# Optimization experiments

Measured on AMD Instinct MI355X. Metric: run time of the kernel, lower is better.

The kernel has to match this reference:

```python
import jax, jax.numpy as jnp
import numpy as np

B, S, D, H = 16, 1024, 768, 12
HD = D // H
SCALE = HD ** -0.5


def setup_inputs() -> dict:
    key = jax.random.key(0)
    k1, k2, k3, k4 = jax.random.split(key, 4)
    # Xavier-uniform-like init for the linear weights
    lim_qkv = (6.0 / (D + 3 * D)) ** 0.5
    lim_proj = (6.0 / (D + D)) ** 0.5
    return {
        "hidden_states": jax.random.normal(k1, (B, S, D), dtype=jnp.float32),
        "mask": jax.random.randint(k2, (B, S), 0, 2).astype(bool),
        "qkv_w": jax.random.uniform(k3, (3 * D, D), minval=-lim_qkv, maxval=lim_qkv, dtype=jnp.float32),
        "qkv_b": jnp.zeros((3 * D,), dtype=jnp.float32),
        "proj_w": jax.random.uniform(k4, (D, D), minval=-lim_proj, maxval=lim_proj, dtype=jnp.float32),
        "proj_b": jnp.zeros((D,), dtype=jnp.float32),
    }


def _masked_softmax(scores, attn_mask):
    # scores: [B,H,S,S]; attn_mask: [B,1,S,S] bool. Fully-masked rows -> all-zero
    # weights (torch gives NaN there but then zeroes the output rows; zeroing
    # the weights yields the identical final output without NaNs).
    neg_inf = jnp.finfo(scores.dtype).min
    m = jnp.max(jnp.where(attn_mask, scores, neg_inf), axis=-1, keepdims=True)
    e = jnp.where(attn_mask, jnp.exp(scores - m), 0.0)
    denom = jnp.sum(e, axis=-1, keepdims=True)
    return e / jnp.where(denom == 0, 1.0, denom)


def reference(hidden_states, mask, qkv_w, qkv_b, proj_w, proj_b):
    # fused QKV projection: [B,S,3D]
    qkv = hidden_states @ qkv_w.T + qkv_b
    qkv = qkv.reshape(B, S, 3, H, HD).transpose(2, 0, 3, 1, 4)  # [3,B,H,S,hd]
    q, k, v = qkv[0], qkv[1], qkv[2]
    tok_mask = mask[:, None, :, None]  # [B,1,S,1]
    q = jnp.where(tok_mask, q, 0.0)
    k = jnp.where(tok_mask, k, 0.0)
    v = jnp.where(tok_mask, v, 0.0)
    scores = jnp.einsum("bhqd,bhkd->bhqk", q, k) * SCALE
    attn_mask = (mask[:, :, None] & mask[:, None, :])[:, None]  # [B,1,S,S]
    attn = _masked_softmax(scores, attn_mask)
    context = jnp.einsum("bhqk,bhkd->bhqd", attn, v)
    context = context.transpose(0, 2, 1, 3).reshape(B, S, D)
    out = context @ proj_w.T + proj_b
    out = jnp.where(mask[:, :, None], out, 0.0)
    return out
```

## Files before the change

kernel.cpp:

```cpp
#include <hip/hip_runtime.h>
#include <cstdint>
#include <cstddef>

#define B 16
#define S 1024
#define D 768
#define H 12
#define HD 64
#define NTOK (B * S)
#define QKV_N (3 * D)
#define SCALE 0.125f
#define C2 2.88539008f
#define GK 768
#define NT_K 12

typedef _Float16 f16x8 __attribute__((ext_vector_type(8)));
typedef _Float16 f16x4 __attribute__((ext_vector_type(4)));
typedef __fp16 fp16x2 __attribute__((ext_vector_type(2)));
typedef float f32x4 __attribute__((ext_vector_type(4)));

typedef __attribute__((address_space(3))) void as3_void;
typedef const __attribute__((address_space(1))) void as1_void;

#if defined(__has_builtin)
#if __has_builtin(__builtin_amdgcn_exp2f)
#define EXP2(x) __builtin_amdgcn_exp2f(x)
#else
#define EXP2(x) exp2f(x)
#endif
#else
#define EXP2(x) exp2f(x)
#endif

__global__ __launch_bounds__(256) void normalize_mask_kernel(
    const unsigned char* __restrict__ raw, int* __restrict__ outm, int n) {
    __shared__ int s_isbyte;
    const int tid = threadIdx.x;
    if (tid == 0) s_isbyte = 0;
    __syncthreads();
    int found = 0;
    for (int i = tid; i < n; i += 256) {
        if ((i & 3) != 0 && raw[i] != 0) found = 1;
    }
    if (found) atomicOr(&s_isbyte, 1);
    __syncthreads();
    const int isbyte = s_isbyte;
    if (isbyte) {
        for (int i = tid; i < n; i += 256) outm[i] = raw[i] ? 1 : 0;
    } else {
        const int* r32 = (const int*)raw;
        for (int i = tid; i < n; i += 256) outm[i] = r32[i] ? 1 : 0;
    }
}

__global__ __launch_bounds__(256) void cvt_all_f16(
    const float* __restrict__ in0, _Float16* __restrict__ out0, int n0,
    const float* __restrict__ in1, _Float16* __restrict__ out1, int n1,
    const float* __restrict__ in2, _Float16* __restrict__ out2, int n2) {
    int i = blockIdx.x * 256 + threadIdx.x;
    const float* in;
    _Float16* out;
    if (i < n0) { in = in0; out = out0; }
    else if (i < n0 + n1) { i -= n0; in = in1; out = out1; }
    else { i -= n0 + n1; in = in2; out = out2; if (i >= n2) return; }
    const float4 v = ((const float4*)in)[i];
    f16x4 o;
    o[0] = (_Float16)v.x; o[1] = (_Float16)v.y;
    o[2] = (_Float16)v.z; o[3] = (_Float16)v.w;
    ((f16x4*)out)[i] = o;
}

template <int MODE>
__global__ __launch_bounds__(256, 2) void gemm16(
    const _Float16* __restrict__ A, const _Float16* __restrict__ Wm,
    const float* __restrict__ bias, const int* __restrict__ rowmask,
    int N, float* __restrict__ outf, _Float16* __restrict__ outh,
    _Float16* __restrict__ vtb) {
    __shared__ _Float16 smem[32768];

    const int tid = threadIdx.x;
    const int w = tid >> 6, l = tid & 63;
    const int wm = (w >> 1) * 64, wn = (w & 1) * 64;
    const int lg = l >> 4, lc = l & 15;

    const int bid = blockIdx.x;
    const int xcd = bid & 7;
    const int idx = bid >> 3;
    const int bn = (idx >> 4) * 128;
    const int bm = (xcd * 16 + (idx & 15)) * 128;

    f32x4 acc[4][4] = {};

#define STAGE(T, BUF)                                                           \
    {                                                                           \
        const int kt_ = (T) * 64;                                               \
        _Pragma("unroll")                                                       \
        for (int i_ = 0; i_ < 4; ++i_) {                                        \
            const int ci_ = (w << 2) + i_;                           \
            const int r_ = (ci_ << 3) + (l >> 3);                               \
            const int c16_ = (l & 7) ^ (r_ & 7);                                \
            __builtin_amdgcn_global_load_lds(                                   \
                (as1_void*)(A + (size_t)(bm + r_) * GK + kt_ + c16_ * 8),       \
                (as3_void*)(smem + (BUF) * 8192 + ci_ * 512), 16, 0, 0);        \
            __builtin_amdgcn_global_load_lds(                                   \
                (as1_void*)(Wm + (size_t)(bn + r_) * GK + kt_ + c16_ * 8),      \
                (as3_void*)(smem + 16384 + (BUF) * 8192 + ci_ * 512), 16, 0, 0);\
        }                                                                       \
    }

    STAGE(0, 0)

    for (int t = 0; t < NT_K; ++t) {
        const int cur = t & 1;
        if (t + 1 < NT_K) {
            STAGE(t + 1, cur ^ 1)
            asm volatile("s_waitcnt vmcnt(8)" ::: "memory");
        } else {
            asm volatile("s_waitcnt vmcnt(0)" ::: "memory");
        }
        __builtin_amdgcn_s_barrier();

        const _Float16* sA = smem + cur * 8192;
        const _Float16* sB = smem + 16384 + cur * 8192;
        __builtin_amdgcn_s_setprio(1);
#pragma unroll
        for (int kk = 0; kk < 2; ++kk) {
            const int c16 = ((kk << 2) + lg) ^ (lc & 7);
            f16x8 af[4], bf[4];
#pragma unroll
            for (int ni = 0; ni < 4; ++ni)
                bf[ni] = *(const f16x8*)&sB[(wn + ni * 16 + lc) * 64 + c16 * 8];
#pragma unroll
            for (int mi = 0; mi < 4; ++mi)
                af[mi] = *(const f16x8*)&sA[(wm + mi * 16 + lc) * 64 + c16 * 8];
#pragma unroll
            for (int mi = 0; mi < 4; ++mi)
#pragma unroll
                for (int ni = 0; ni < 4; ++ni)
                    acc[mi][ni] = __builtin_amdgcn_mfma_f32_16x16x32_f16(
                        af[mi], bf[ni], acc[mi][ni], 0, 0, 0);
        }
        __builtin_amdgcn_s_setprio(0);
        __builtin_amdgcn_s_barrier();
    }
#undef STAGE

    float bs[4];
#pragma unroll
    for (int ni = 0; ni < 4; ++ni) bs[ni] = bias[bn + wn + ni * 16 + lc];

    if (MODE == 1) {
        if (bn < 1536) {
#pragma unroll
            for (int mi = 0; mi < 4; ++mi) {
#pragma unroll
                for (int j = 0; j < 4; ++j) {
                    const int m = bm + wm + mi * 16 + lg * 4 + j;
#pragma unroll
                    for (int ni = 0; ni < 4; ++ni) {
                        const int col = bn + wn + ni * 16 + lc;
                        outh[(size_t)m * N + col] =
                            (_Float16)(acc[mi][ni][j] + bs[ni]);
                    }
                }
            }
        } else {
#pragma unroll
            for (int mi = 0; mi < 4; ++mi) {
#pragma unroll
                for (int ni = 0; ni < 4; ++ni) {
                    f16x4 v4;
#pragma unroll
                    for (int j = 0; j < 4; ++j)
                        v4[j] = (_Float16)(acc[mi][ni][j] + bs[ni]);
                    const int nl = wn + ni * 16 + lc;
                    const int ml = wm + mi * 16 + lg * 4;
                    *(f16x4*)&smem[nl * 136 + ml] = v4;
                }
            }
            __syncthreads();
            const int r = tid >> 1;
            const int c0 = (tid & 1) * 64;
            const int col0 = bn - 1536 + r;
            const int hh = col0 >> 6, hd = col0 & 63;
            const int bb = bm >> 10;
            const int s0 = (bm & 1023) + c0;
            _Float16* dst = vtb + ((size_t)(bb * H + hh) * HD + hd) * S + s0;
#pragma unroll
            for (int e = 0; e < 8; ++e)
                *(f16x8*)(dst + e * 8) = *(const f16x8*)&smem[r * 136 + c0 + e * 8];
        }
    } else {
#pragma unroll
        for (int mi = 0; mi < 4; ++mi) {
#pragma unroll
            for (int j = 0; j < 4; ++j) {
                const int m = bm + wm + mi * 16 + lg * 4 + j;
                const int mv = rowmask[m];
#pragma unroll
                for (int ni = 0; ni < 4; ++ni) {
                    const int col = bn + wn + ni * 16 + lc;
                    outf[(size_t)m * N + col] = mv ? acc[mi][ni][j] + bs[ni] : 0.f;
                }
            }
        }
    }
}

__global__ __launch_bounds__(256, 3) void attn_kernel(
    const _Float16* __restrict__ qkv, const _Float16* __restrict__ vtb,
    const int* __restrict__ mask, _Float16* __restrict__ ctx) {
    __shared__ _Float16 ksm[2][64 * 64];
    __shared__ _Float16 vsm[2][64 * 64];
    __shared__ float mbias[S];

    const int blk = blockIdx.x;
    const int xcd = blk & 7;
    const int idx = blk >> 3;
    const int bh_ = xcd * 24 + (idx >> 2);
    const int qt = idx & 3;
    const int h = bh_ % H;
    const int b = bh_ / H;
    const int tid = threadIdx.x;
    const int w = tid >> 6, lane = tid & 63;
    const int lg = lane >> 4, lc = lane & 15;

    const size_t bh = (size_t)(b * H + h);
    const _Float16* Kp = qkv + (size_t)(b * S) * QKV_N + D + h * HD;
    const _Float16* Vt = vtb + bh * HD * S;
    const int* mrow = mask + b * S;

    const int r0 = w * 8 + (lane >> 3);
    const int swz8 = ((lane & 7) ^ (r0 & 7)) * 8;
    const int koff0 = r0 * QKV_N + swz8;
    const int koff1 = (32 + r0) * QKV_N + swz8;
    const int voff0 = r0 * S + swz8;
    const int voff1 = (32 + r0) * S + swz8;

#define STAGE(KT, BUF)                                                         \
    {                                                                          \
        __builtin_amdgcn_global_load_lds(                                      \
            (as1_void*)(Kp + (size_t)(KT) * QKV_N + koff0),                    \
            (as3_void*)(&ksm[BUF][w * 512]), 16, 0, 0);                        \
        __builtin_amdgcn_global_load_lds(                                      \
            (as1_void*)(Kp + (size_t)(KT) * QKV_N + koff1),                    \
            (as3_void*)(&ksm[BUF][2048 + w * 512]), 16, 0, 0);                 \
        __builtin_amdgcn_global_load_lds(                                      \
            (as1_void*)(Vt + (size_t)(KT) + voff0),                            \
            (as3_void*)(&vsm[BUF][w * 512]), 16, 0, 0);                        \
        __builtin_amdgcn_global_load_lds(                                      \
            (as1_void*)(Vt + (size_t)(KT) + voff1),                            \
            (as3_void*)(&vsm[BUF][2048 + w * 512]), 16, 0, 0);                 \
    }

    const int qbase = qt * 256 + w * 16 + lc;
    const _Float16 qs = (_Float16)(0.125f * 1.44269504f);
    f16x8 qf[4][2];
#pragma unroll
    for (int qg = 0; qg < 4; ++qg) {
        const _Float16* Qp =
            qkv + (size_t)(b * S + qbase + qg * 64) * QKV_N + h * HD;
        qf[qg][0] = *(const f16x8*)(Qp + lg * 8);
        qf[qg][1] = *(const f16x8*)(Qp + 32 + lg * 8);
        qf[qg][0] *= qs;
        qf[qg][1] *= qs;
    }

#pragma unroll
    for (int i = 0; i < 4; ++i)
        mbias[i * 256 + tid] = mrow[i * 256 + tid] ? -C2 : -1e9f;

    STAGE(0, 0)
    __syncthreads();

    f32x4 acc[4][4] = {};
    float lsum[4] = {0.f, 0.f, 0.f, 0.f};
    fp16x2 ones;
    ones[0] = (__fp16)1.0f; ones[1] = (__fp16)1.0f;

    for (int it = 0; it < S / 64; ++it) {
        const int cur = it & 1;
        if (it + 1 < S / 64) STAGE((it + 1) * 64, cur ^ 1)

        __builtin_amdgcn_s_setprio(1);
#pragma unroll
        for (int t = 0; t < 4; ++t) {
            const int krow = (t * 16 + lc) * 64;
            const f16x8 kfa =
                *(const f16x8*)&ksm[cur][krow + (lg ^ (lc & 7)) * 8];
            const f16x8 kfb =
                *(const f16x8*)&ksm[cur][krow + ((4 + lg) ^ (lc & 7)) * 8];
            const f32x4 mb = *(const f32x4*)&mbias[it * 64 + t * 16 + 4 * lg];

            f16x4 pp[4];
#pragma unroll
            for (int qg = 0; qg < 4; ++qg) {
                f32x4 c = mb;
                c = __builtin_amdgcn_mfma_f32_16x16x32_f16(kfa, qf[qg][0], c, 0, 0, 0);
                c = __builtin_amdgcn_mfma_f32_16x16x32_f16(kfb, qf[qg][1], c, 0, 0, 0);
                const auto u0 = __builtin_amdgcn_cvt_pkrtz(EXP2(c[0]), EXP2(c[1]));
                const auto u1 = __builtin_amdgcn_cvt_pkrtz(EXP2(c[2]), EXP2(c[3]));
                lsum[qg] = __builtin_amdgcn_fdot2(u0, ones, lsum[qg], false);
                lsum[qg] = __builtin_amdgcn_fdot2(u1, ones, lsum[qg], false);
                pp[qg][0] = (_Float16)u0[0]; pp[qg][1] = (_Float16)u0[1];
                pp[qg][2] = (_Float16)u1[0]; pp[qg][3] = (_Float16)u1[1];
            }

#pragma unroll
            for (int g = 0; g < 4; ++g) {
                const int vrow = (g * 16 + lc) * 64;
                const f16x4 vf = *(const f16x4*)&vsm[cur][
                    vrow + (((2 * t + (lg >> 1)) ^ (lc & 7)) << 3) + (lg & 1) * 4];
#pragma unroll
                for (int qg = 0; qg < 4; ++qg)
                    acc[qg][g] = __builtin_amdgcn_mfma_f32_16x16x16f16(
                        pp[qg], vf, acc[qg][g], 0, 0, 0);
            }
        }
        __builtin_amdgcn_s_setprio(0);
        __syncthreads();
    }
#undef STAGE

#pragma unroll
    for (int qg = 0; qg < 4; ++qg) {
        float l = lsum[qg];
        l += __shfl_xor(l, 16);
        l += __shfl_xor(l, 32);
        const float inv = l > 0.f ? 1.f / l : 0.f;
#pragma unroll
        for (int j = 0; j < 4; ++j) {
            const int qin = 4 * lg + j;
            const float ij = __shfl(inv, qin);
            const int qr = qt * 256 + qg * 64 + w * 16 + qin;
            const float iq = mrow[qr] ? ij : 0.f;
            const size_t o = ((size_t)(b * S + qr)) * D + h * HD;
#pragma unroll
            for (int g = 0; g < 4; ++g)
                ctx[o + 16 * g + lc] = (_Float16)(acc[qg][g][j] * iq);
        }
    }
}

extern "C" void kernel_launch(void* const* d_in, const int* in_sizes, int n_in,
                              void* d_out, int out_size, void* d_ws, size_t ws_size,
                              hipStream_t stream) {
    const float* hidden = (const float*)d_in[0];
    const unsigned char* maskraw = (const unsigned char*)d_in[1];
    const float* qkv_w = (const float*)d_in[2];
    const float* qkv_b = (const float*)d_in[3];
    const float* proj_w = (const float*)d_in[4];
    const float* proj_b = (const float*)d_in[5];
    float* out = (float*)d_out;

    char* ws = (char*)d_ws;
    size_t off = 0;
    int* maskN = (int*)(ws + off);            off += (size_t)NTOK * 4;
    _Float16* hid16 = (_Float16*)(ws + off);  off += (size_t)NTOK * D * 2;
    _Float16* qkvw16 = (_Float16*)(ws + off); off += (size_t)QKV_N * D * 2;
    _Float16* projw16 = (_Float16*)(ws + off); off += (size_t)D * D * 2;
    _Float16* qkv16 = (_Float16*)(ws + off);  off += (size_t)NTOK * QKV_N * 2;
    _Float16* vt = (_Float16*)(ws + off);     off += (size_t)NTOK * D * 2;
    _Float16* ctx16 = (_Float16*)(ws + off);  off += (size_t)NTOK * D * 2;

    normalize_mask_kernel<<<1, 256, 0, stream>>>(maskraw, maskN, NTOK);

    const int n0 = NTOK * D / 4, n1 = QKV_N * D / 4, n2 = D * D / 4;
    cvt_all_f16<<<(n0 + n1 + n2 + 255) / 256, 256, 0, stream>>>(
        hidden, hid16, n0, qkv_w, qkvw16, n1, proj_w, projw16, n2);

    gemm16<1><<<dim3(2304), 256, 0, stream>>>(
        hid16, qkvw16, qkv_b, nullptr, QKV_N, nullptr, qkv16, vt);

    attn_kernel<<<dim3(B * H * (S / 256)), 256, 0, stream>>>(qkv16, vt, maskN, ctx16);

    gemm16<0><<<dim3(768), 256, 0, stream>>>(
        ctx16, projw16, proj_b, maskN, D, out, nullptr, nullptr);
}
```

Measured before the change: 206.7 us.

## Triple-buffer K/V tiles in attention with explicit vmcnt waits

Moves the attention kernel's K/V shared-memory staging from double to triple buffering. It prefetches two tiles ahead and replaces __syncthreads with explicit s_waitcnt vmcnt levels plus raw s_barrier, so more global-load latency overlaps the MFMA work. The GEMM barriers also switch to inline-asm s_barrier. The cost is an extra 16KB of LDS per block, which may reduce occupancy under launch_bounds(256,3), and hand-tuned waitcnt counts that must match the number of loads in flight.

```diff
diff --git a/kernel.cpp b/kernel.cpp
--- a/kernel.cpp
+++ b/kernel.cpp
@@ -31,6 +31,8 @@
 #else
 #define EXP2(x) exp2f(x)
 #endif
+
+#define BARRIER() asm volatile("s_barrier" ::: "memory")
 
 __global__ __launch_bounds__(256) void normalize_mask_kernel(
     const unsigned char* __restrict__ raw, int* __restrict__ outm, int n) {
@@ -118,7 +120,7 @@
         } else {
             asm volatile("s_waitcnt vmcnt(0)" ::: "memory");
         }
-        __builtin_amdgcn_s_barrier();
+        BARRIER();
 
         const _Float16* sA = smem + cur * 8192;
         const _Float16* sB = smem + 16384 + cur * 8192;
@@ -141,7 +143,7 @@
                         af[mi], bf[ni], acc[mi][ni], 0, 0, 0);
         }
         __builtin_amdgcn_s_setprio(0);
-        __builtin_amdgcn_s_barrier();
+        BARRIER();
     }
 #undef STAGE
 
@@ -210,8 +212,8 @@
 __global__ __launch_bounds__(256, 3) void attn_kernel(
     const _Float16* __restrict__ qkv, const _Float16* __restrict__ vtb,
     const int* __restrict__ mask, _Float16* __restrict__ ctx) {
-    __shared__ _Float16 ksm[2][64 * 64];
-    __shared__ _Float16 vsm[2][64 * 64];
+    __shared__ _Float16 ksm[3][64 * 64];
+    __shared__ _Float16 vsm[3][64 * 64];
     __shared__ float mbias[S];
 
     const int blk = blockIdx.x;
@@ -237,19 +239,20 @@
     const int voff0 = r0 * S + swz8;
     const int voff1 = (32 + r0) * S + swz8;
 
-#define STAGE(KT, BUF)                                                         \
+#define STAGE(T, BUF)                                                          \
     {                                                                          \
+        const int kt_ = (T) * 64;                                              \
         __builtin_amdgcn_global_load_lds(                                      \
-            (as1_void*)(Kp + (size_t)(KT) * QKV_N + koff0),                    \
+            (as1_void*)(Kp + (size_t)kt_ * QKV_N + koff0),                     \
             (as3_void*)(&ksm[BUF][w * 512]), 16, 0, 0);                        \
         __builtin_amdgcn_global_load_lds(                                      \
-            (as1_void*)(Kp + (size_t)(KT) * QKV_N + koff1),                    \
+            (as1_void*)(Kp + (size_t)kt_ * QKV_N + koff1),                     \
             (as3_void*)(&ksm[BUF][2048 + w * 512]), 16, 0, 0);                 \
         __builtin_amdgcn_global_load_lds(                                      \
-            (as1_void*)(Vt + (size_t)(KT) + voff0),                            \
+            (as1_void*)(Vt + (size_t)kt_ + voff0),                            \
             (as3_void*)(&vsm[BUF][w * 512]), 16, 0, 0);                        \
         __builtin_amdgcn_global_load_lds(                                      \
-            (as1_void*)(Vt + (size_t)(KT) + voff1),                            \
+            (as1_void*)(Vt + (size_t)kt_ + voff1),                            \
             (as3_void*)(&vsm[BUF][2048 + w * 512]), 16, 0, 0);                 \
     }
 
@@ -271,16 +274,28 @@
         mbias[i * 256 + tid] = mrow[i * 256 + tid] ? -C2 : -1e9f;
 
     STAGE(0, 0)
-    __syncthreads();
+    STAGE(1, 1)
 
     f32x4 acc[4][4] = {};
     float lsum[4] = {0.f, 0.f, 0.f, 0.f};
     fp16x2 ones;
     ones[0] = (__fp16)1.0f; ones[1] = (__fp16)1.0f;
 
+    int cur = 0;
     for (int it = 0; it < S / 64; ++it) {
-        const int cur = it & 1;
-        if (it + 1 < S / 64) STAGE((it + 1) * 64, cur ^ 1)
+        if (it + 2 < S / 64) {
+            int nb = cur + 2; if (nb >= 3) nb -= 3;
+            STAGE(it + 2, nb)
+        }
+        if (it == 0)
+            asm volatile("s_waitcnt vmcnt(8) lgkmcnt(0)" ::: "memory");
+        else if (it + 2 < S / 64)
+            asm volatile("s_waitcnt vmcnt(8)" ::: "memory");
+        else if (it + 2 == S / 64)
+            asm volatile("s_waitcnt vmcnt(4)" ::: "memory");
+        else
+            asm volatile("s_waitcnt vmcnt(0)" ::: "memory");
+        BARRIER();
 
         __builtin_amdgcn_s_setprio(1);
 #pragma unroll
@@ -318,7 +333,8 @@
             }
         }
         __builtin_amdgcn_s_setprio(0);
-        __syncthreads();
+        BARRIER();
+        if (++cur >= 3) cur = 0;
     }
 #undef STAGE
 
```

Measured after the change: 200.1 us. 3.2% less time.
